# Optimization experiments

Hardware: AMD Instinct MI355X
Metric: run time of the kernel (lower is better)

## Reference

```python
import jax, jax.numpy as jnp
import numpy as np

D = 512
F = 2048
H = 8
L = 128
B = 4


def _layer_norm(x, g, b, eps=1e-5):
    mu = jnp.mean(x, axis=-1, keepdims=True)
    var = jnp.var(x, axis=-1, keepdims=True)
    return (x - mu) * jax.lax.rsqrt(var + eps) * g + b


def _edge_mlp(Q, arc, W, b, arc_is_middle_out):
    # Equivalent to relu(Linear(concat(A, arc, B_))) with W: (3D, D), without
    # materializing the (B,L,L,3D) concat: split W into three D-blocks.
    # For W_out: concat(h_bf, arc, h_bf_t) -> block1 acts on Q[b,i], block3 on Q[b,j].
    # For W_in:  concat(h_bf_t, arc, h_bf) -> block1 acts on Q[b,j], block3 on Q[b,i].
    d = Q.shape[-1]
    W1, W2, W3 = W[:d], W[d:2 * d], W[2 * d:]
    mid = jnp.einsum('bijd,de->bije', arc, W2)
    if arc_is_middle_out:  # W_out ordering
        left = jnp.einsum('bid,de->bie', Q, W1)[:, :, None, :]   # broadcast over j
        right = jnp.einsum('bjd,de->bje', Q, W3)[:, None, :, :]  # broadcast over i
    else:  # W_in ordering
        left = jnp.einsum('bjd,de->bje', Q, W1)[:, None, :, :]
        right = jnp.einsum('bid,de->bie', Q, W3)[:, :, None, :]
    return jax.nn.relu(left + mid + right + b)


def _gat_attn(Q, KV, q_w, q_b, k_w, k_b, v_w, v_b, o_w, o_b):
    # Edge-conditioned multihead attention: per-query K/V of shape (B,L,L,D).
    bsz, seq, d = Q.shape
    dh = d // H
    scale = dh ** -0.5
    q = ((Q @ q_w + q_b) * scale).reshape(bsz, seq, H, dh)
    k = (KV @ k_w + k_b).reshape(bsz, seq, seq, H, dh)
    v = (KV @ v_w + v_b).reshape(bsz, seq, seq, H, dh)
    scores = jnp.einsum('bihd,bijhd->bhij', q, k)
    attn = jax.nn.softmax(scores, axis=-1)
    out = jnp.einsum('bhij,bijhd->bihd', attn, v).reshape(bsz, seq, d)
    return out @ o_w + o_b


def setup_inputs() -> dict:
    key = jax.random.key(0)
    ks = jax.random.split(key, 24)
    s = 0.02
    inp = {
        'h': jax.random.normal(ks[0], (L, B, D), jnp.float32),
        'src_outcoming_arc_x': jax.random.normal(ks[1], (B, L, L, D), jnp.float32),
        'src_incoming_arc_x': jax.random.normal(ks[2], (B, L, L, D), jnp.float32),
        'encoder_padding_mask': jnp.zeros((B, L), jnp.bool_),
        'W_out_w': jax.random.normal(ks[3], (3 * D, D), jnp.float32) * s,
        'W_out_b': jnp.zeros((D,), jnp.float32),
        'W_in_w': jax.random.normal(ks[4], (3 * D, D), jnp.float32) * s,
        'W_in_b': jnp.zeros((D,), jnp.float32),
        'q_w': jax.random.normal(ks[5], (D, D), jnp.float32) * s,
        'q_b': jnp.zeros((D,), jnp.float32),
        'k_w': jax.random.normal(ks[6], (D, D), jnp.float32) * s,
        'k_b': jnp.zeros((D,), jnp.float32),
        'v_w': jax.random.normal(ks[7], (D, D), jnp.float32) * s,
        'v_b': jnp.zeros((D,), jnp.float32),
        'o_w': jax.random.normal(ks[8], (D, D), jnp.float32) * s,
        'o_b': jnp.zeros((D,), jnp.float32),
        'ln1_g': jnp.ones((D,), jnp.float32),
        'ln1_b': jnp.zeros((D,), jnp.float32),
        'fc1_w': jax.random.normal(ks[9], (D, F), jnp.float32) * s,
        'fc1_b': jnp.zeros((F,), jnp.float32),
        'fc2_w': jax.random.normal(ks[10], (F, D), jnp.float32) * s,
        'fc2_b': jnp.zeros((D,), jnp.float32),
        'ln2_g': jnp.ones((D,), jnp.float32),
        'ln2_b': jnp.zeros((D,), jnp.float32),
    }
    return inp


def reference(h, src_outcoming_arc_x, src_incoming_arc_x, encoder_padding_mask,
              W_out_w, W_out_b, W_in_w, W_in_b,
              q_w, q_b, k_w, k_b, v_w, v_b, o_w, o_b,
              ln1_g, ln1_b, fc1_w, fc1_b, fc2_w, fc2_b, ln2_g, ln2_b):
    # h: (L, B, D). Dropouts are identity (eval). attn_mask=None.
    residual = h
    Q = jnp.transpose(h, (1, 0, 2))  # (B, L, D)
    U_out = _edge_mlp(Q, src_outcoming_arc_x, W_out_w, W_out_b, True)
    att_out = _gat_attn(Q, U_out, q_w, q_b, k_w, k_b, v_w, v_b, o_w, o_b)
    U_in = _edge_mlp(Q, src_incoming_arc_x, W_in_w, W_in_b, False)
    att_in = _gat_attn(Q, U_in, q_w, q_b, k_w, k_b, v_w, v_b, o_w, o_b)
    x = jnp.transpose(att_in + att_out, (1, 0, 2))  # back to (L, B, D)
    x = _layer_norm(residual + x, ln1_g, ln1_b)
    residual = x
    x = jax.nn.relu(x @ fc1_w + fc1_b) @ fc2_w + fc2_b
    x = _layer_norm(residual + x, ln2_g, ln2_b)
    return x
```

## Files before the change

kernel.cpp:

```cpp
#include <hip/hip_runtime.h>
#include <stdint.h>
#include <stddef.h>

#define NTOK 512
#define NM   65536

typedef __bf16 bf16x8 __attribute__((ext_vector_type(8)));
typedef float  f32x4  __attribute__((ext_vector_type(4)));
typedef unsigned int u32x4 __attribute__((ext_vector_type(4)));

__device__ __forceinline__ unsigned short f2bf(float f) {
    unsigned int u = __builtin_bit_cast(unsigned int, f);
    u += 0x7FFFu + ((u >> 16) & 1u);
    return (unsigned short)(u >> 16);
}
__device__ __forceinline__ float bf2f(unsigned short s) {
    unsigned int u = ((unsigned int)s) << 16;
    return __builtin_bit_cast(float, u);
}

__global__ __launch_bounds__(256) void k_qtrans(const float* __restrict__ h,
                                                unsigned short* __restrict__ Qm) {
    int idx = blockIdx.x * 256 + threadIdx.x;
    int tok = idx >> 9, d = idx & 511;
    int b = tok >> 7, i = tok & 127;
    Qm[idx] = f2bf(h[(i * 4 + b) * 512 + d]);
}

struct TRJob { const float* src; unsigned short* dst; int srcLd, dstLd, tcols; float scale; };
struct TRJobs { TRJob j[11]; int start[12]; };

__global__ __launch_bounds__(256) void k_trN(TRJobs js) {
    __shared__ float tile[64][65];
    int b = blockIdx.x;
    int ji = 0;
    while (ji < 10 && b >= js.start[ji + 1]) ++ji;
    TRJob jb = js.j[ji];
    int rel = b - js.start[ji];
    int bx = rel % jb.tcols, by = rel / jb.tcols;
    int r0 = by * 64, c0 = bx * 64;
    int t = threadIdx.x;
    int c = t & 63, rr = t >> 6;
    #pragma unroll
    for (int ii = 0; ii < 16; ++ii) {
        int r = ii * 4 + rr;
        tile[r][c] = jb.src[(size_t)(r0 + r) * jb.srcLd + c0 + c];
    }
    __syncthreads();
    #pragma unroll
    for (int ii = 0; ii < 16; ++ii) {
        int n = ii * 4 + rr;
        jb.dst[(size_t)(c0 + n) * jb.dstLd + r0 + c] = f2bf(tile[c][n] * jb.scale);
    }
}

__global__ __launch_bounds__(256) void k_kwT(const float* __restrict__ kw,
                                             float* __restrict__ kwT) {
    int idx = blockIdx.x * 256 + threadIdx.x;
    kwT[idx] = kw[(size_t)(idx & 511) * 512 + (idx >> 9)];
}
__global__ __launch_bounds__(256) void k_bias1(const float* __restrict__ Wob,
                                               const float* __restrict__ Wib,
                                               const float* __restrict__ qb,
                                               float* __restrict__ bias1) {
    int i = blockIdx.x * 256 + threadIdx.x;
    if (i >= 2560) return;
    float v = 0.f;
    if (i < 512) v = Wob[i];
    else if (i < 1024) v = 0.f;
    else if (i < 1536) v = Wib[i - 1024];
    else if (i < 2048) v = 0.f;
    else v = qb[i - 2048] * 0.125f;
    bias1[i] = v;
}

struct MMP {
    const unsigned short* A;  int lda;
    const unsigned short* Bt; int ldb;
    const float* bias;
    const float* accs;
    float* outF;
    unsigned short* outB;
    int ldo;
    int K;
    int relu;
    int aOffPerN64;
    int zKOff;
    int zOutOff;
};

__global__ __launch_bounds__(256) void k_mm(MMP p) {
    __shared__ unsigned char As[64 * 128];
    __shared__ unsigned char Bs[64 * 128];
    int t = threadIdx.x;
    int lane = t & 63, w = t >> 6;
    int m0 = blockIdx.x * 64, n0 = blockIdx.y * 64;
    int z = blockIdx.z;
    const unsigned short* A  = p.A + (size_t)(n0 >> 6) * p.aOffPerN64 + (size_t)z * p.zKOff;
    const unsigned short* Bt = p.Bt + (size_t)z * p.zKOff;
    int wm = (w >> 1) * 32, wn = (w & 1) * 32;
    f32x4 acc[2][2];
    #pragma unroll
    for (int a = 0; a < 2; ++a)
        #pragma unroll
        for (int b = 0; b < 2; ++b) acc[a][b] = (f32x4){0.f, 0.f, 0.f, 0.f};

    for (int kb = 0; kb < p.K; kb += 64) {
        __syncthreads();
        #pragma unroll
        for (int s = 0; s < 2; ++s) {
            int c = t + s * 256;
            int r = c >> 3, kc = (c & 7) * 8;
            int off = (r * 128 + kc * 2) ^ ((r & 7) << 4);
            *reinterpret_cast<u32x4*>(As + off) =
                *reinterpret_cast<const u32x4*>(A + (size_t)(m0 + r) * p.lda + kb + kc);
            *reinterpret_cast<u32x4*>(Bs + off) =
                *reinterpret_cast<const u32x4*>(Bt + (size_t)(n0 + r) * p.ldb + kb + kc);
        }
        __syncthreads();
        #pragma unroll
        for (int kh = 0; kh < 2; ++kh) {
            int kk = kh * 32 + (lane >> 4) * 8;
            bf16x8 af[2], bfr[2];
            #pragma unroll
            for (int mf = 0; mf < 2; ++mf) {
                int r = wm + mf * 16 + (lane & 15);
                int off = (r * 128 + kk * 2) ^ ((r & 7) << 4);
                af[mf] = *reinterpret_cast<const bf16x8*>(As + off);
            }
            #pragma unroll
            for (int nf = 0; nf < 2; ++nf) {
                int r = wn + nf * 16 + (lane & 15);
                int off = (r * 128 + kk * 2) ^ ((r & 7) << 4);
                bfr[nf] = *reinterpret_cast<const bf16x8*>(Bs + off);
            }
            #pragma unroll
            for (int mf = 0; mf < 2; ++mf)
                #pragma unroll
                for (int nf = 0; nf < 2; ++nf)
                    acc[mf][nf] = __builtin_amdgcn_mfma_f32_16x16x32_bf16(
                        af[mf], bfr[nf], acc[mf][nf], 0, 0, 0);
        }
    }
    #pragma unroll
    for (int mf = 0; mf < 2; ++mf) {
        #pragma unroll
        for (int rr = 0; rr < 4; ++rr) {
            int gm = m0 + wm + mf * 16 + (lane >> 4) * 4 + rr;
            #pragma unroll
            for (int nf = 0; nf < 2; ++nf) {
                int e = n0 + wn + nf * 16 + (lane & 15);
                float v = acc[mf][nf][rr];
                if (p.bias) v += p.bias[e];
                if (p.relu) v = fmaxf(v, 0.f);
                if (p.accs) v += p.accs[(size_t)gm * p.ldo + e];
                size_t oo = (size_t)gm * p.ldo + e + (size_t)z * p.zOutOff;
                if (p.outF) p.outF[oo] = v;
                if (p.outB) p.outB[oo] = f2bf(v);
            }
        }
    }
}

__global__ __launch_bounds__(256) void k_prep2(const float* __restrict__ qs, int qld,
                                               const float* __restrict__ kwT,
                                               const float* __restrict__ k_b,
                                               unsigned short* __restrict__ p,
                                               float* __restrict__ c) {
    __shared__ float q8[8][512];
    int t = threadIdx.x;
    int tok0 = blockIdx.x * 8;
    int d = blockIdx.y * 256 + t;
    for (int idx = t; idx < 4096; idx += 256) {
        int s = idx >> 9, dd = idx & 511;
        q8[s][dd] = qs[(size_t)(tok0 + s) * qld + dd];
    }
    __syncthreads();
    if (blockIdx.y == 0 && t < 64) {
        int s = t >> 3, hh = t & 7;
        float cv = 0.f;
        for (int dh = 0; dh < 64; ++dh) cv += k_b[hh * 64 + dh] * q8[s][hh * 64 + dh];
        c[(tok0 + s) * 8 + hh] = cv;
    }
    for (int hh = 0; hh < 8; ++hh) {
        float pv[8];
        #pragma unroll
        for (int s = 0; s < 8; ++s) pv[s] = 0.f;
        for (int dh = 0; dh < 64; ++dh) {
            float wv = kwT[(size_t)(hh * 64 + dh) * 512 + d];
            #pragma unroll
            for (int s = 0; s < 8; ++s) pv[s] += wv * q8[s][hh * 64 + dh];
        }
        #pragma unroll
        for (int s = 0; s < 8; ++s)
            p[((size_t)(tok0 + s) * 8 + hh) * 512 + d] = f2bf(pv[s]);
    }
}

__global__ __launch_bounds__(256) void k_midU(const float* __restrict__ arc,
                                              const unsigned short* __restrict__ W2t,
                                              const float* __restrict__ fixedMat, int fld,
                                              const float* __restrict__ rowMat, int rld,
                                              unsigned short* __restrict__ U) {
    __shared__ unsigned char As[128 * 64 * 2];
    __shared__ unsigned char Bs[128 * 64 * 2];
    int t = threadIdx.x;
    int lane = t & 63;
    int w = t >> 6;
    int bid = blockIdx.x;
    int xcd = bid & 7, slot = bid >> 3;
    int mt = xcd * 64 + (slot >> 2);
    int nt = slot & 3;
    int m0 = mt * 128;
    int n0 = nt * 128;
    int wm = (w >> 1) * 64, wn = (w & 1) * 64;
    f32x4 acc[4][4];
    #pragma unroll
    for (int a = 0; a < 4; ++a)
        #pragma unroll
        for (int bq = 0; bq < 4; ++bq) acc[a][bq] = (f32x4){0.f, 0.f, 0.f, 0.f};

    for (int kb = 0; kb < 512; kb += 64) {
        __syncthreads();
        #pragma unroll
        for (int sc4 = 0; sc4 < 4; ++sc4) {
            int chunk = t + sc4 * 256;
            int r = chunk >> 3, kc = (chunk & 7) * 8;
            const float4* srcA = reinterpret_cast<const float4*>(
                arc + (size_t)(m0 + r) * 512 + kb + kc);
            float4 f0 = srcA[0], f1 = srcA[1];
            bf16x8 bv;
            bv[0] = (__bf16)f0.x; bv[1] = (__bf16)f0.y;
            bv[2] = (__bf16)f0.z; bv[3] = (__bf16)f0.w;
            bv[4] = (__bf16)f1.x; bv[5] = (__bf16)f1.y;
            bv[6] = (__bf16)f1.z; bv[7] = (__bf16)f1.w;
            int off = (r * 128 + kc * 2) ^ ((r & 7) << 4);
            *reinterpret_cast<bf16x8*>(As + off) = bv;
            *reinterpret_cast<u32x4*>(Bs + off) =
                *reinterpret_cast<const u32x4*>(W2t + (size_t)(n0 + r) * 512 + kb + kc);
        }
        __syncthreads();
        #pragma unroll
        for (int kh = 0; kh < 2; ++kh) {
            int kk = kh * 32 + (lane >> 4) * 8;
            bf16x8 af[4], bfr[4];
            #pragma unroll
            for (int mf = 0; mf < 4; ++mf) {
                int r = wm + mf * 16 + (lane & 15);
                int off = (r * 128 + kk * 2) ^ ((r & 7) << 4);
                af[mf] = *reinterpret_cast<const bf16x8*>(As + off);
            }
            #pragma unroll
            for (int nf = 0; nf < 4; ++nf) {
                int r = wn + nf * 16 + (lane & 15);
                int off = (r * 128 + kk * 2) ^ ((r & 7) << 4);
                bfr[nf] = *reinterpret_cast<const bf16x8*>(Bs + off);
            }
            #pragma unroll
            for (int mf = 0; mf < 4; ++mf)
                #pragma unroll
                for (int nf = 0; nf < 4; ++nf)
                    acc[mf][nf] = __builtin_amdgcn_mfma_f32_16x16x32_bf16(
                        af[mf], bfr[nf], acc[mf][nf], 0, 0, 0);
        }
    }
    int tokI = mt;
    int bb = mt >> 7;
    float fx[4];
    #pragma unroll
    for (int nf = 0; nf < 4; ++nf)
        fx[nf] = fixedMat[(size_t)tokI * fld + n0 + wn + nf * 16 + (lane & 15)];
    #pragma unroll
    for (int mf = 0; mf < 4; ++mf) {
        #pragma unroll
        for (int r = 0; r < 4; ++r) {
            int row = wm + mf * 16 + (lane >> 4) * 4 + r;
            int gm = m0 + row;
            int tokJ = bb * 128 + (gm & 127);
            const float* rv = rowMat + (size_t)tokJ * rld;
            #pragma unroll
            for (int nf = 0; nf < 4; ++nf) {
                int e = n0 + wn + nf * 16 + (lane & 15);
                float v = acc[mf][nf][r] + fx[nf] + rv[e];
                v = fmaxf(v, 0.f);
                U[(size_t)gm * 512 + e] = f2bf(v);
            }
        }
    }
}

__global__ __launch_bounds__(256) void k_scores(const unsigned short* __restrict__ U,
                                                const unsigned short* __restrict__ p,
                                                const float* __restrict__ c,
                                                float* __restrict__ attn) {
    __shared__ float sc[8][128];
    int tok = blockIdx.x;
    int t = threadIdx.x;
    int w = t >> 6;
    int lane = t & 63;
    int hh = lane & 15;
    int kg = lane >> 4;
    bool hv = hh < 8;
    f32x4 acc[2];
    acc[0] = (f32x4){0.f, 0.f, 0.f, 0.f};
    acc[1] = (f32x4){0.f, 0.f, 0.f, 0.f};
    const unsigned short* Ub = U + (size_t)tok * 65536 + (size_t)(w * 32) * 512;
    const unsigned short* pb = p + ((size_t)tok * 8 + (hh & 7)) * 512;
    for (int ks = 0; ks < 16; ++ks) {
        int kcol = ks * 32 + kg * 8;
        u32x4 braw = (u32x4){0u, 0u, 0u, 0u};
        if (hv) braw = *reinterpret_cast<const u32x4*>(pb + kcol);
        bf16x8 bfrag = __builtin_bit_cast(bf16x8, braw);
        #pragma unroll
        for (int mf = 0; mf < 2; ++mf) {
            bf16x8 afrag = *reinterpret_cast<const bf16x8*>(
                Ub + (size_t)(mf * 16 + hh) * 512 + kcol);
            acc[mf] = __builtin_amdgcn_mfma_f32_16x16x32_bf16(afrag, bfrag, acc[mf], 0, 0, 0);
        }
    }
    if (hv) {
        float cval = c[tok * 8 + hh];
        #pragma unroll
        for (int mf = 0; mf < 2; ++mf)
            #pragma unroll
            for (int r = 0; r < 4; ++r)
                sc[hh][w * 32 + mf * 16 + kg * 4 + r] = acc[mf][r] + cval;
    }
    __syncthreads();
    int h2 = t >> 5, l32 = t & 31;
    float v0 = sc[h2][l32], v1 = sc[h2][l32 + 32],
          v2 = sc[h2][l32 + 64], v3 = sc[h2][l32 + 96];
    float mx = fmaxf(fmaxf(v0, v1), fmaxf(v2, v3));
    #pragma unroll
    for (int o = 16; o >= 1; o >>= 1) mx = fmaxf(mx, __shfl_xor(mx, o));
    float e0 = __expf(v0 - mx), e1 = __expf(v1 - mx),
          e2 = __expf(v2 - mx), e3 = __expf(v3 - mx);
    float sum = e0 + e1 + e2 + e3;
    #pragma unroll
    for (int o = 16; o >= 1; o >>= 1) sum += __shfl_xor(sum, o);
    float inv = 1.f / sum;
    float* ab = attn + (size_t)tok * 1024 + h2 * 128;
    ab[l32]      = e0 * inv;
    ab[l32 + 32] = e1 * inv;
    ab[l32 + 64] = e2 * inv;
    ab[l32 + 96] = e3 * inv;
}

__global__ __launch_bounds__(256) void k_wacc(const unsigned short* __restrict__ U,
                                              const float* __restrict__ attn,
                                              unsigned short* __restrict__ Wacc) {
    __shared__ float at[1024];
    int t = threadIdx.x;
    int tok = blockIdx.x;
    for (int idx = t; idx < 1024; idx += 256) at[idx] = attn[(size_t)tok * 1024 + idx];
    __syncthreads();
    int d0 = t * 2;
    const unsigned short* Ub = U + (size_t)tok * 65536;
    float acc[8][2];
    #pragma unroll
    for (int hh = 0; hh < 8; ++hh) { acc[hh][0] = 0.f; acc[hh][1] = 0.f; }
    for (int j = 0; j < 128; ++j) {
        unsigned int uv = *reinterpret_cast<const unsigned int*>(Ub + (size_t)j * 512 + d0);
        float u0 = bf2f((unsigned short)(uv & 0xffffu));
        float u1 = bf2f((unsigned short)(uv >> 16));
        #pragma unroll
        for (int hh = 0; hh < 8; ++hh) {
            float a = at[hh * 128 + j];
            acc[hh][0] += a * u0;
            acc[hh][1] += a * u1;
        }
    }
    #pragma unroll
    for (int hh = 0; hh < 8; ++hh) {
        unsigned short* wp = Wacc + ((size_t)tok * 8 + hh) * 512 + d0;
        wp[0] = f2bf(acc[hh][0]);
        wp[1] = f2bf(acc[hh][1]);
    }
}

__global__ __launch_bounds__(256) void k_ln(const float* __restrict__ A,
                                            const float* __restrict__ Bv, int bswap,
                                            const float* __restrict__ parts,
                                            const float* __restrict__ pbias,
                                            const float* __restrict__ g,
                                            const float* __restrict__ bta,
                                            float* __restrict__ outF,
                                            unsigned short* __restrict__ outB) {
    int t = threadIdx.x;
    int tok = blockIdx.x;
    size_t aoff = (size_t)tok * 512;
    float b0, b1;
    if (parts) {
        b0 = parts[aoff + t] + parts[262144 + aoff + t] +
             parts[524288 + aoff + t] + parts[786432 + aoff + t] + pbias[t];
        b1 = parts[aoff + t + 256] + parts[262144 + aoff + t + 256] +
             parts[524288 + aoff + t + 256] + parts[786432 + aoff + t + 256] + pbias[t + 256];
    } else {
        size_t boff = aoff;
        if (bswap) { int i = tok >> 2, b = tok & 3; boff = (size_t)(b * 128 + i) * 512; }
        b0 = Bv[boff + t];
        b1 = Bv[boff + t + 256];
    }
    float v0 = A[aoff + t] + b0;
    float v1 = A[aoff + t + 256] + b1;
    float s = v0 + v1, q = v0 * v0 + v1 * v1;
    #pragma unroll
    for (int o = 32; o >= 1; o >>= 1) { s += __shfl_xor(s, o); q += __shfl_xor(q, o); }
    __shared__ float red[8];
    int w = t >> 6, lane = t & 63;
    if (lane == 0) { red[w] = s; red[4 + w] = q; }
    __syncthreads();
    float ts = red[0] + red[1] + red[2] + red[3];
    float tq = red[4] + red[5] + red[6] + red[7];
    float mean = ts * (1.f / 512.f);
    float var = tq * (1.f / 512.f) - mean * mean;
    float inv = rsqrtf(var + 1e-5f);
    float o0 = (v0 - mean) * inv * g[t] + bta[t];
    float o1 = (v1 - mean) * inv * g[t + 256] + bta[t + 256];
    outF[aoff + t] = o0;
    outF[aoff + t + 256] = o1;
    if (outB) { outB[aoff + t] = f2bf(o0); outB[aoff + t + 256] = f2bf(o1); }
}

extern "C" void kernel_launch(void* const* d_in, const int* in_sizes, int n_in,
                              void* d_out, int out_size, void* d_ws, size_t ws_size,
                              hipStream_t stream) {
    (void)in_sizes; (void)n_in; (void)out_size; (void)ws_size;
    const float* h       = (const float*)d_in[0];
    const float* arc_out = (const float*)d_in[1];
    const float* arc_in  = (const float*)d_in[2];
    const float* W_out_w = (const float*)d_in[4];
    const float* W_out_b = (const float*)d_in[5];
    const float* W_in_w  = (const float*)d_in[6];
    const float* W_in_b  = (const float*)d_in[7];
    const float* q_w  = (const float*)d_in[8];
    const float* q_b  = (const float*)d_in[9];
    const float* k_w  = (const float*)d_in[10];
    const float* k_b  = (const float*)d_in[11];
    const float* v_w  = (const float*)d_in[12];
    const float* v_b  = (const float*)d_in[13];
    const float* o_w  = (const float*)d_in[14];
    const float* o_b  = (const float*)d_in[15];
    const float* ln1_g = (const float*)d_in[16];
    const float* ln1_b = (const float*)d_in[17];
    const float* fc1_w = (const float*)d_in[18];
    const float* fc1_b = (const float*)d_in[19];
    const float* fc2_w = (const float*)d_in[20];
    const float* fc2_b = (const float*)d_in[21];
    const float* ln2_g = (const float*)d_in[22];
    const float* ln2_b = (const float*)d_in[23];
    float* out = (float*)d_out;

    char* wsb = (char*)d_ws;
    size_t off = 0;
    auto ALLOC = [&](size_t bytes) -> void* {
        void* ptr = wsb + off;
        off += (bytes + 255) & ~(size_t)255;
        return ptr;
    };
    unsigned short* WcatT = (unsigned short*)ALLOC((size_t)2560 * 512 * 2);
    unsigned short* W2to  = (unsigned short*)ALLOC(262144 * 2);
    unsigned short* W2ti  = (unsigned short*)ALLOC(262144 * 2);
    unsigned short* o_wT  = (unsigned short*)ALLOC(262144 * 2);
    unsigned short* v_wT  = (unsigned short*)ALLOC(262144 * 2);
    unsigned short* fc1T  = (unsigned short*)ALLOC((size_t)2048 * 512 * 2);
    unsigned short* fc2T  = (unsigned short*)ALLOC((size_t)512 * 2048 * 2);
    float* kwT   = (float*)ALLOC(262144 * 4);
    float* bias1 = (float*)ALLOC(2560 * 4);
    unsigned short* Qm = (unsigned short*)ALLOC(262144 * 2);
    float* QWcat = (float*)ALLOC((size_t)512 * 2560 * 4);
    unsigned short* pbuf = (unsigned short*)ALLOC((size_t)NTOK * 8 * 512 * 2);
    float* cbuf = (float*)ALLOC(NTOK * 8 * 4);
    unsigned short* Ubuf = (unsigned short*)ALLOC((size_t)NM * 512 * 2);
    float* attnb = (float*)ALLOC((size_t)NTOK * 8 * 128 * 4);
    unsigned short* Waccb = (unsigned short*)ALLOC((size_t)NTOK * 8 * 512 * 2);
    unsigned short* tmpb  = (unsigned short*)ALLOC(262144 * 2);
    float* attsum = (float*)ALLOC(262144 * 4);
    float* x1  = (float*)ALLOC(262144 * 4);
    unsigned short* x1b = (unsigned short*)ALLOC(262144 * 2);
    unsigned short* ybb = (unsigned short*)ALLOC((size_t)NTOK * 2048 * 2);
    float* zparts = (float*)ALLOC((size_t)4 * 262144 * 4);

    k_qtrans<<<1024, 256, 0, stream>>>(h, Qm);

    {
        TRJobs js = {};
        auto SET = [&](int i, const float* s, int sld, unsigned short* d, int dld,
                       float sc, int tiles, int tcols) {
            js.j[i] = TRJob{s, d, sld, dld, tcols, sc};
            js.start[i + 1] = js.start[i] + tiles;
        };
        js.start[0] = 0;
        SET(0,  W_out_w,              512, WcatT,              512, 1.f,    64, 8);
        SET(1,  W_out_w + 1024 * 512, 512, WcatT + 512 * 512,  512, 1.f,    64, 8);
        SET(2,  W_in_w,               512, WcatT + 1024 * 512, 512, 1.f,    64, 8);
        SET(3,  W_in_w + 1024 * 512,  512, WcatT + 1536 * 512, 512, 1.f,    64, 8);
        SET(4,  q_w,                  512, WcatT + 2048 * 512, 512, 0.125f, 64, 8);
        SET(5,  W_out_w + 512 * 512,  512, W2to,               512, 1.f,    64, 8);
        SET(6,  W_in_w + 512 * 512,   512, W2ti,               512, 1.f,    64, 8);
        SET(7,  o_w,                  512, o_wT,               512, 1.f,    64, 8);
        SET(8,  v_w,                  512, v_wT,               512, 1.f,    64, 8);
        SET(9,  fc1_w,               2048, fc1T,               512, 1.f,   256, 32);
        SET(10, fc2_w,                512, fc2T,              2048, 1.f,   256, 8);
        k_trN<<<js.start[11], 256, 0, stream>>>(js);
    }
    k_kwT<<<1024, 256, 0, stream>>>(k_w, kwT);
    k_bias1<<<10, 256, 0, stream>>>(W_out_b, W_in_b, q_b, bias1);

    {
        MMP m = {};
        m.A = Qm; m.lda = 512; m.Bt = WcatT; m.ldb = 512;
        m.bias = bias1; m.outF = QWcat; m.ldo = 2560; m.K = 512;
        k_mm<<<dim3(8, 40), 256, 0, stream>>>(m);
    }
    k_prep2<<<dim3(64, 2), 256, 0, stream>>>(QWcat + 2048, 2560, kwT, k_b, pbuf, cbuf);

    for (int arc = 0; arc < 2; ++arc) {
        const float* arcp = (arc == 0) ? arc_out : arc_in;
        const unsigned short* w2 = (arc == 0) ? W2to : W2ti;
        const float* fixedM = (arc == 0) ? QWcat + 0    : QWcat + 1536;
        const float* rowM   = (arc == 0) ? QWcat + 512  : QWcat + 1024;
        k_midU<<<2048, 256, 0, stream>>>(arcp, w2, fixedM, 2560, rowM, 2560, Ubuf);
        k_scores<<<512, 256, 0, stream>>>(Ubuf, pbuf, cbuf, attnb);
        k_wacc<<<512, 256, 0, stream>>>(Ubuf, attnb, Waccb);
        {
            MMP m = {};
            m.A = Waccb; m.lda = 4096; m.aOffPerN64 = 512;
            m.Bt = v_wT; m.ldb = 512;
            m.bias = v_b; m.outB = tmpb; m.ldo = 512; m.K = 512;
            k_mm<<<dim3(8, 8), 256, 0, stream>>>(m);
        }
        {
            MMP m = {};
            m.A = tmpb; m.lda = 512; m.Bt = o_wT; m.ldb = 512;
            m.bias = o_b; m.outF = attsum; m.ldo = 512; m.K = 512;
            m.accs = (arc == 0) ? nullptr : attsum;
            k_mm<<<dim3(8, 8), 256, 0, stream>>>(m);
        }
    }

    k_ln<<<512, 256, 0, stream>>>(h, attsum, 1, nullptr, nullptr, ln1_g, ln1_b, x1, x1b);

    {
        MMP m = {};
        m.A = x1b; m.lda = 512; m.Bt = fc1T; m.ldb = 512;
        m.bias = fc1_b; m.relu = 1; m.outB = ybb; m.ldo = 2048; m.K = 512;
        k_mm<<<dim3(8, 32), 256, 0, stream>>>(m);
    }
    {
        MMP m = {};
        m.A = ybb; m.lda = 2048; m.Bt = fc2T; m.ldb = 2048;
        m.outF = zparts; m.ldo = 512; m.K = 512;
        m.zKOff = 512; m.zOutOff = 262144;
        k_mm<<<dim3(8, 8, 4), 256, 0, stream>>>(m);
    }
    k_ln<<<512, 256, 0, stream>>>(x1, nullptr, 0, zparts, fc2_b, ln2_g, ln2_b, out, nullptr);
}
```

Measured before the change: 398.3 us.

## Prefetch midU tiles into registers and fuse scores/softmax/weighted-sum into one kernel

The k_midU GEMM loop now issues global loads for the next K-block into registers before computing on the current one. This overlaps the fp32 arc loads with the MFMA work, and raw s_barrier calls replace the __syncthreads pair. The k_scores and k_wacc kernels are merged into one k_att kernel with 512 threads. It stages each token's 128x512 bf16 U tile in 128KB of swizzled LDS once, then computes scores, softmax and the attention-weighted sum from shared memory. This removes the second global read of U and the attn buffer round-trip, at the cost of heavy LDS use that limits occupancy to one block per CU.

```diff
diff --git a/kernel.cpp b/kernel.cpp
--- a/kernel.cpp
+++ b/kernel.cpp
@@ -220,26 +220,41 @@
         #pragma unroll
         for (int bq = 0; bq < 4; ++bq) acc[a][bq] = (f32x4){0.f, 0.f, 0.f, 0.f};
 
-    for (int kb = 0; kb < 512; kb += 64) {
-        __syncthreads();
+    float4 pfA0[4], pfA1[4];
+    u32x4 pfB[4];
+    #define ISSUE(KB)                                                              \
+        _Pragma("unroll")                                                          \
+        for (int sc4 = 0; sc4 < 4; ++sc4) {                                        \
+            int chunk = t + sc4 * 256;                                             \
+            int r = chunk >> 3, kc = (chunk & 7) * 8;                              \
+            const float4* srcA = reinterpret_cast<const float4*>(                  \
+                arc + (size_t)(m0 + r) * 512 + (KB) + kc);                         \
+            pfA0[sc4] = srcA[0];                                                   \
+            pfA1[sc4] = srcA[1];                                                   \
+            pfB[sc4] = *reinterpret_cast<const u32x4*>(                            \
+                W2t + (size_t)(n0 + r) * 512 + (KB) + kc);                         \
+        }
+
+    ISSUE(0);
+    for (int kb8 = 0; kb8 < 8; ++kb8) {
         #pragma unroll
         for (int sc4 = 0; sc4 < 4; ++sc4) {
             int chunk = t + sc4 * 256;
             int r = chunk >> 3, kc = (chunk & 7) * 8;
-            const float4* srcA = reinterpret_cast<const float4*>(
-                arc + (size_t)(m0 + r) * 512 + kb + kc);
-            float4 f0 = srcA[0], f1 = srcA[1];
             bf16x8 bv;
-            bv[0] = (__bf16)f0.x; bv[1] = (__bf16)f0.y;
-            bv[2] = (__bf16)f0.z; bv[3] = (__bf16)f0.w;
-            bv[4] = (__bf16)f1.x; bv[5] = (__bf16)f1.y;
-            bv[6] = (__bf16)f1.z; bv[7] = (__bf16)f1.w;
+            bv[0] = (__bf16)pfA0[sc4].x; bv[1] = (__bf16)pfA0[sc4].y;
+            bv[2] = (__bf16)pfA0[sc4].z; bv[3] = (__bf16)pfA0[sc4].w;
+            bv[4] = (__bf16)pfA1[sc4].x; bv[5] = (__bf16)pfA1[sc4].y;
+            bv[6] = (__bf16)pfA1[sc4].z; bv[7] = (__bf16)pfA1[sc4].w;
             int off = (r * 128 + kc * 2) ^ ((r & 7) << 4);
             *reinterpret_cast<bf16x8*>(As + off) = bv;
-            *reinterpret_cast<u32x4*>(Bs + off) =
-                *reinterpret_cast<const u32x4*>(W2t + (size_t)(n0 + r) * 512 + kb + kc);
-        }
-        __syncthreads();
+            *reinterpret_cast<u32x4*>(Bs + off) = pfB[sc4];
+        }
+        asm volatile("s_waitcnt lgkmcnt(0)" ::: "memory");
+        __builtin_amdgcn_sched_barrier(0);
+        __builtin_amdgcn_s_barrier();
+        __builtin_amdgcn_sched_barrier(0);
+        if (kb8 < 7) { ISSUE((kb8 + 1) * 64); }
         #pragma unroll
         for (int kh = 0; kh < 2; ++kh) {
             int kk = kh * 32 + (lane >> 4) * 8;
@@ -263,7 +278,12 @@
                     acc[mf][nf] = __builtin_amdgcn_mfma_f32_16x16x32_bf16(
                         af[mf], bfr[nf], acc[mf][nf], 0, 0, 0);
         }
-    }
+        asm volatile("s_waitcnt lgkmcnt(0)" ::: "memory");
+        __builtin_amdgcn_sched_barrier(0);
+        __builtin_amdgcn_s_barrier();
+        __builtin_amdgcn_sched_barrier(0);
+    }
+    #undef ISSUE
     int tokI = mt;
     int bb = mt >> 7;
     float fx[4];
@@ -289,93 +309,79 @@
     }
 }
 
-__global__ __launch_bounds__(256) void k_scores(const unsigned short* __restrict__ U,
-                                                const unsigned short* __restrict__ p,
-                                                const float* __restrict__ c,
-                                                float* __restrict__ attn) {
+__global__ __launch_bounds__(512) void k_att(const unsigned short* __restrict__ U,
+                                             const unsigned short* __restrict__ p,
+                                             const float* __restrict__ c,
+                                             unsigned short* __restrict__ Wacc) {
+    __shared__ unsigned char Us[128 * 1024];
     __shared__ float sc[8][128];
     int tok = blockIdx.x;
     int t = threadIdx.x;
-    int w = t >> 6;
-    int lane = t & 63;
-    int hh = lane & 15;
-    int kg = lane >> 4;
+    int w = t >> 6, lane = t & 63;
+    const unsigned short* Ug = U + (size_t)tok * 65536;
+    #pragma unroll
+    for (int it = 0; it < 16; ++it) {
+        int r = it * 8 + w;
+        int cc = lane * 16;
+        u32x4 v = *reinterpret_cast<const u32x4*>(
+            reinterpret_cast<const unsigned char*>(Ug) + (size_t)r * 1024 + cc);
+        *reinterpret_cast<u32x4*>(Us + (((r * 1024 + cc)) ^ ((r & 7) << 4))) = v;
+    }
+    __syncthreads();
+    int hh = lane & 15, kg = lane >> 4;
     bool hv = hh < 8;
-    f32x4 acc[2];
-    acc[0] = (f32x4){0.f, 0.f, 0.f, 0.f};
-    acc[1] = (f32x4){0.f, 0.f, 0.f, 0.f};
-    const unsigned short* Ub = U + (size_t)tok * 65536 + (size_t)(w * 32) * 512;
+    f32x4 acc = (f32x4){0.f, 0.f, 0.f, 0.f};
     const unsigned short* pb = p + ((size_t)tok * 8 + (hh & 7)) * 512;
     for (int ks = 0; ks < 16; ++ks) {
         int kcol = ks * 32 + kg * 8;
         u32x4 braw = (u32x4){0u, 0u, 0u, 0u};
         if (hv) braw = *reinterpret_cast<const u32x4*>(pb + kcol);
         bf16x8 bfrag = __builtin_bit_cast(bf16x8, braw);
-        #pragma unroll
-        for (int mf = 0; mf < 2; ++mf) {
-            bf16x8 afrag = *reinterpret_cast<const bf16x8*>(
-                Ub + (size_t)(mf * 16 + hh) * 512 + kcol);
-            acc[mf] = __builtin_amdgcn_mfma_f32_16x16x32_bf16(afrag, bfrag, acc[mf], 0, 0, 0);
-        }
+        int row = w * 16 + hh;
+        bf16x8 afrag = *reinterpret_cast<const bf16x8*>(
+            Us + ((row * 1024 + kcol * 2) ^ ((row & 7) << 4)));
+        acc = __builtin_amdgcn_mfma_f32_16x16x32_bf16(afrag, bfrag, acc, 0, 0, 0);
     }
     if (hv) {
         float cval = c[tok * 8 + hh];
         #pragma unroll
-        for (int mf = 0; mf < 2; ++mf)
-            #pragma unroll
-            for (int r = 0; r < 4; ++r)
-                sc[hh][w * 32 + mf * 16 + kg * 4 + r] = acc[mf][r] + cval;
+        for (int r = 0; r < 4; ++r)
+            sc[hh][w * 16 + kg * 4 + r] = acc[r] + cval;
     }
     __syncthreads();
-    int h2 = t >> 5, l32 = t & 31;
-    float v0 = sc[h2][l32], v1 = sc[h2][l32 + 32],
-          v2 = sc[h2][l32 + 64], v3 = sc[h2][l32 + 96];
-    float mx = fmaxf(fmaxf(v0, v1), fmaxf(v2, v3));
-    #pragma unroll
-    for (int o = 16; o >= 1; o >>= 1) mx = fmaxf(mx, __shfl_xor(mx, o));
-    float e0 = __expf(v0 - mx), e1 = __expf(v1 - mx),
-          e2 = __expf(v2 - mx), e3 = __expf(v3 - mx);
-    float sum = e0 + e1 + e2 + e3;
-    #pragma unroll
-    for (int o = 16; o >= 1; o >>= 1) sum += __shfl_xor(sum, o);
-    float inv = 1.f / sum;
-    float* ab = attn + (size_t)tok * 1024 + h2 * 128;
-    ab[l32]      = e0 * inv;
-    ab[l32 + 32] = e1 * inv;
-    ab[l32 + 64] = e2 * inv;
-    ab[l32 + 96] = e3 * inv;
-}
-
-__global__ __launch_bounds__(256) void k_wacc(const unsigned short* __restrict__ U,
-                                              const float* __restrict__ attn,
-                                              unsigned short* __restrict__ Wacc) {
-    __shared__ float at[1024];
-    int t = threadIdx.x;
-    int tok = blockIdx.x;
-    for (int idx = t; idx < 1024; idx += 256) at[idx] = attn[(size_t)tok * 1024 + idx];
+    if (t < 256) {
+        int h2 = t >> 5, l32 = t & 31;
+        float v0 = sc[h2][l32], v1 = sc[h2][l32 + 32],
+              v2 = sc[h2][l32 + 64], v3 = sc[h2][l32 + 96];
+        float mx = fmaxf(fmaxf(v0, v1), fmaxf(v2, v3));
+        #pragma unroll
+        for (int o = 16; o >= 1; o >>= 1) mx = fmaxf(mx, __shfl_xor(mx, o));
+        float e0 = __expf(v0 - mx), e1 = __expf(v1 - mx),
+              e2 = __expf(v2 - mx), e3 = __expf(v3 - mx);
+        float sum = e0 + e1 + e2 + e3;
+        #pragma unroll
+        for (int o = 16; o >= 1; o >>= 1) sum += __shfl_xor(sum, o);
+        float inv = 1.f / sum;
+        sc[h2][l32]      = e0 * inv;
+        sc[h2][l32 + 32] = e1 * inv;
+        sc[h2][l32 + 64] = e2 * inv;
+        sc[h2][l32 + 96] = e3 * inv;
+    }
     __syncthreads();
-    int d0 = t * 2;
-    const unsigned short* Ub = U + (size_t)tok * 65536;
-    float acc[8][2];
-    #pragma unroll
-    for (int hh = 0; hh < 8; ++hh) { acc[hh][0] = 0.f; acc[hh][1] = 0.f; }
+    float av0 = sc[w][lane], av1 = sc[w][lane + 64];
+    float accd[8];
+    #pragma unroll
+    for (int i = 0; i < 8; ++i) accd[i] = 0.f;
     for (int j = 0; j < 128; ++j) {
-        unsigned int uv = *reinterpret_cast<const unsigned int*>(Ub + (size_t)j * 512 + d0);
-        float u0 = bf2f((unsigned short)(uv & 0xffffu));
-        float u1 = bf2f((unsigned short)(uv >> 16));
-        #pragma unroll
-        for (int hh = 0; hh < 8; ++hh) {
-            float a = at[hh * 128 + j];
-            acc[hh][0] += a * u0;
-            acc[hh][1] += a * u1;
-        }
-    }
-    #pragma unroll
-    for (int hh = 0; hh < 8; ++hh) {
-        unsigned short* wp = Wacc + ((size_t)tok * 8 + hh) * 512 + d0;
-        wp[0] = f2bf(acc[hh][0]);
-        wp[1] = f2bf(acc[hh][1]);
-    }
+        float aj = (j < 64) ? __shfl(av0, j) : __shfl(av1, j - 64);
+        bf16x8 uv = *reinterpret_cast<const bf16x8*>(
+            Us + ((j * 1024 + lane * 16) ^ ((j & 7) << 4)));
+        #pragma unroll
+        for (int i = 0; i < 8; ++i) accd[i] += aj * (float)uv[i];
+    }
+    unsigned short* wp = Wacc + ((size_t)tok * 8 + w) * 512 + lane * 8;
+    #pragma unroll
+    for (int i = 0; i < 8; ++i) wp[i] = f2bf(accd[i]);
 }
 
 __global__ __launch_bounds__(256) void k_ln(const float* __restrict__ A,
@@ -472,7 +478,6 @@
     unsigned short* pbuf = (unsigned short*)ALLOC((size_t)NTOK * 8 * 512 * 2);
     float* cbuf = (float*)ALLOC(NTOK * 8 * 4);
     unsigned short* Ubuf = (unsigned short*)ALLOC((size_t)NM * 512 * 2);
-    float* attnb = (float*)ALLOC((size_t)NTOK * 8 * 128 * 4);
     unsigned short* Waccb = (unsigned short*)ALLOC((size_t)NTOK * 8 * 512 * 2);
     unsigned short* tmpb  = (unsigned short*)ALLOC(262144 * 2);
     float* attsum = (float*)ALLOC(262144 * 4);
@@ -521,8 +526,7 @@
         const float* fixedM = (arc == 0) ? QWcat + 0    : QWcat + 1536;
         const float* rowM   = (arc == 0) ? QWcat + 512  : QWcat + 1024;
         k_midU<<<2048, 256, 0, stream>>>(arcp, w2, fixedM, 2560, rowM, 2560, Ubuf);
-        k_scores<<<512, 256, 0, stream>>>(Ubuf, pbuf, cbuf, attnb);
-        k_wacc<<<512, 256, 0, stream>>>(Ubuf, attnb, Waccb);
+        k_att<<<512, 512, 0, stream>>>(Ubuf, pbuf, cbuf, Waccb);
         {
             MMP m = {};
             m.A = Waccb; m.lda = 4096; m.aOffPerN64 = 512;
```

Result: slower. 445.8 us (+11.9%).

## Double-buffer LDS tiles in k_midU with register prefetch of next K-slice

Applied to the files above, without the earlier changes.

The edge-MLP middle GEMM kernel now keeps two LDS buffers and loads the next K-slice of arc and W2t into registers while MFMAs run on the current buffer. The converted data is then written to the alternate buffer, leaving one barrier per iteration instead of two. The goal is to hide global memory latency behind compute. In exchange it doubles LDS use to 64KB per block and adds prefetch registers, which may lower occupancy.

```diff
diff --git a/kernel.cpp b/kernel.cpp
--- a/kernel.cpp
+++ b/kernel.cpp
@@ -202,8 +202,8 @@
                                               const float* __restrict__ fixedMat, int fld,
                                               const float* __restrict__ rowMat, int rld,
                                               unsigned short* __restrict__ U) {
-    __shared__ unsigned char As[128 * 64 * 2];
-    __shared__ unsigned char Bs[128 * 64 * 2];
+    __shared__ unsigned short As[2][128 * 64];
+    __shared__ unsigned short Bs[2][128 * 64];
     int t = threadIdx.x;
     int lane = t & 63;
     int w = t >> 6;
@@ -211,8 +211,7 @@
     int xcd = bid & 7, slot = bid >> 3;
     int mt = xcd * 64 + (slot >> 2);
     int nt = slot & 3;
-    int m0 = mt * 128;
-    int n0 = nt * 128;
+    int m0 = mt * 128, n0 = nt * 128;
     int wm = (w >> 1) * 64, wn = (w & 1) * 64;
     f32x4 acc[4][4];
     #pragma unroll
@@ -220,41 +219,57 @@
         #pragma unroll
         for (int bq = 0; bq < 4; ++bq) acc[a][bq] = (f32x4){0.f, 0.f, 0.f, 0.f};
 
-    for (int kb = 0; kb < 512; kb += 64) {
-        __syncthreads();
-        #pragma unroll
-        for (int sc4 = 0; sc4 < 4; ++sc4) {
-            int chunk = t + sc4 * 256;
-            int r = chunk >> 3, kc = (chunk & 7) * 8;
-            const float4* srcA = reinterpret_cast<const float4*>(
-                arc + (size_t)(m0 + r) * 512 + kb + kc);
-            float4 f0 = srcA[0], f1 = srcA[1];
-            bf16x8 bv;
-            bv[0] = (__bf16)f0.x; bv[1] = (__bf16)f0.y;
-            bv[2] = (__bf16)f0.z; bv[3] = (__bf16)f0.w;
-            bv[4] = (__bf16)f1.x; bv[5] = (__bf16)f1.y;
-            bv[6] = (__bf16)f1.z; bv[7] = (__bf16)f1.w;
-            int off = (r * 128 + kc * 2) ^ ((r & 7) << 4);
-            *reinterpret_cast<bf16x8*>(As + off) = bv;
-            *reinterpret_cast<u32x4*>(Bs + off) =
-                *reinterpret_cast<const u32x4*>(W2t + (size_t)(n0 + r) * 512 + kb + kc);
-        }
-        __syncthreads();
+    int r0t = t >> 3, ct = t & 7;
+    float4 pA0[4], pA1[4];
+    u32x4 pB[4];
+
+#define LOADK(KB)                                                               \
+    _Pragma("unroll")                                                           \
+    for (int j = 0; j < 4; ++j) {                                               \
+        int r = r0t + 32 * j;                                                   \
+        const float* ga = arc + (size_t)(m0 + r) * 512 + (KB) + ct * 8;         \
+        pA0[j] = *reinterpret_cast<const float4*>(ga);                          \
+        pA1[j] = *reinterpret_cast<const float4*>(ga + 4);                      \
+        pB[j] = *reinterpret_cast<const u32x4*>(                                \
+            W2t + (size_t)(n0 + r) * 512 + (KB) + ct * 8);                      \
+    }
+
+#define WRITEK(BUF)                                                             \
+    _Pragma("unroll")                                                           \
+    for (int j = 0; j < 4; ++j) {                                               \
+        int r = r0t + 32 * j;                                                   \
+        int off = (r * 128 + ct * 16) ^ ((r & 7) << 4);                         \
+        bf16x8 bv;                                                              \
+        bv[0] = (__bf16)pA0[j].x; bv[1] = (__bf16)pA0[j].y;                     \
+        bv[2] = (__bf16)pA0[j].z; bv[3] = (__bf16)pA0[j].w;                     \
+        bv[4] = (__bf16)pA1[j].x; bv[5] = (__bf16)pA1[j].y;                     \
+        bv[6] = (__bf16)pA1[j].z; bv[7] = (__bf16)pA1[j].w;                     \
+        *reinterpret_cast<bf16x8*>((char*)As[BUF] + off) = bv;                  \
+        *reinterpret_cast<u32x4*>((char*)Bs[BUF] + off) = pB[j];                \
+    }
+
+    LOADK(0);
+    WRITEK(0);
+    __syncthreads();
+    #pragma unroll
+    for (int kb8 = 0; kb8 < 8; ++kb8) {
+        if (kb8 < 7) LOADK((kb8 + 1) * 64);
+        int cur = kb8 & 1;
         #pragma unroll
         for (int kh = 0; kh < 2; ++kh) {
             int kk = kh * 32 + (lane >> 4) * 8;
             bf16x8 af[4], bfr[4];
             #pragma unroll
             for (int mf = 0; mf < 4; ++mf) {
-                int r = wm + mf * 16 + (lane & 15);
-                int off = (r * 128 + kk * 2) ^ ((r & 7) << 4);
-                af[mf] = *reinterpret_cast<const bf16x8*>(As + off);
+                int rr = wm + mf * 16 + (lane & 15);
+                int off = (rr * 128 + kk * 2) ^ ((rr & 7) << 4);
+                af[mf] = *reinterpret_cast<const bf16x8*>((const char*)As[cur] + off);
             }
             #pragma unroll
             for (int nf = 0; nf < 4; ++nf) {
-                int r = wn + nf * 16 + (lane & 15);
-                int off = (r * 128 + kk * 2) ^ ((r & 7) << 4);
-                bfr[nf] = *reinterpret_cast<const bf16x8*>(Bs + off);
+                int rn = wn + nf * 16 + (lane & 15);
+                int off = (rn * 128 + kk * 2) ^ ((rn & 7) << 4);
+                bfr[nf] = *reinterpret_cast<const bf16x8*>((const char*)Bs[cur] + off);
             }
             #pragma unroll
             for (int mf = 0; mf < 4; ++mf)
@@ -263,7 +278,13 @@
                     acc[mf][nf] = __builtin_amdgcn_mfma_f32_16x16x32_bf16(
                         af[mf], bfr[nf], acc[mf][nf], 0, 0, 0);
         }
-    }
+        if (kb8 < 7) {
+            WRITEK(cur ^ 1);
+            __syncthreads();
+        }
+    }
+#undef LOADK
+#undef WRITEK
     int tokI = mt;
     int bb = mt >> 7;
     float fx[4];
```

Result: no change. 390.7 us (-1.9%).
